# Kernel tuning notes

Measured on AMD Instinct MI355X. Metric: run time of the kernel, lower is better.

Reference implementation:

```python
import jax, jax.numpy as jnp
import numpy as np

DIM = 768
NUM_HEADS = 12
HEAD_DIM = DIM // NUM_HEADS
SCALE = HEAD_DIM ** -0.5


def setup_inputs() -> dict:
    key = jax.random.key(0)
    k1, k2, k3, k4 = jax.random.split(key, 4)
    B, N = 4, 2048
    x = jax.random.normal(k1, (B, N, DIM), dtype=jnp.float32)
    # torch nn.Linear weights: [out_features, in_features]
    w_qkv = jax.random.normal(k2, (3 * DIM, DIM), dtype=jnp.float32) * (DIM ** -0.5)
    w_proj = jax.random.normal(k3, (DIM, DIM), dtype=jnp.float32) * (DIM ** -0.5)
    b_proj = jax.random.normal(k4, (DIM,), dtype=jnp.float32) * 0.01
    return {"x": x, "w_qkv": w_qkv, "w_proj": w_proj, "b_proj": b_proj}


def reference(x, w_qkv, w_proj, b_proj):
    B, N, C = x.shape
    H, D = NUM_HEADS, HEAD_DIM
    qkv = jnp.einsum('bnc,oc->bno', x, w_qkv)              # [B,N,3C]
    qkv = qkv.reshape(B, N, 3, H, D)
    q = qkv[:, :, 0].transpose(0, 2, 1, 3)                 # [B,H,N,D]
    k = qkv[:, :, 1].transpose(0, 2, 1, 3)
    v = qkv[:, :, 2].transpose(0, 2, 1, 3)
    attn = jnp.einsum('bhnd,bhmd->bhnm', q, k) * SCALE     # [B,H,N,N]
    attn = jax.nn.softmax(attn, axis=-1)
    out = jnp.einsum('bhnm,bhmd->bhnd', attn, v)           # [B,H,N,D]
    out = out.transpose(0, 2, 1, 3).reshape(B, N, C)
    return jnp.einsum('bnc,oc->bno', out, w_proj) + b_proj
```

## Files before the change

kernel.cpp:

```cpp
#include <hip/hip_runtime.h>
#include <hip/hip_bf16.h>
#include <cstdint>

typedef _Float16 f16;
typedef __attribute__((ext_vector_type(8))) _Float16 f16x8;
typedef __attribute__((ext_vector_type(4))) _Float16 f16x4;
typedef __attribute__((ext_vector_type(2))) _Float16 f16x2;
typedef __attribute__((ext_vector_type(4))) float f32x4;

#define MFMA(a, b, c) __builtin_amdgcn_mfma_f32_16x16x32_f16((a), (b), (c), 0, 0, 0)
#define MFMA16(a, b, c) __builtin_amdgcn_mfma_f32_16x16x16f16((a), (b), (c), 0, 0, 0)

__device__ static inline void gl_lds16(const void* g, void* l) {
  __builtin_amdgcn_global_load_lds(
      (__attribute__((address_space(1))) const void*)g,
      (__attribute__((address_space(3))) void*)l, 16, 0, 0);
}

__global__ __launch_bounds__(256) void cvt_all(const float* __restrict__ x,
                                               const float* __restrict__ wq,
                                               const float* __restrict__ wp,
                                               f16* __restrict__ xo,
                                               f16* __restrict__ wqo,
                                               f16* __restrict__ wpo) {
  int i = blockIdx.x * 256 + threadIdx.x;
  const float* src;
  f16* dst;
  if (i < 1572864) {
    src = x; dst = xo;
  } else if (i < 1572864 + 442368) {
    i -= 1572864; src = wq; dst = wqo;
  } else {
    i -= 1572864 + 442368;
    if (i >= 147456) return;
    src = wp; dst = wpo;
  }
  const float4 v = reinterpret_cast<const float4*>(src)[i];
  f16x4 o;
  o.x = (f16)v.x; o.y = (f16)v.y; o.z = (f16)v.z; o.w = (f16)v.w;
  reinterpret_cast<f16x4*>(dst)[i] = o;
}

__global__ __launch_bounds__(256) void gemm_qkv(const f16* __restrict__ X,
                                                const f16* __restrict__ W,
                                                f16* __restrict__ Q,
                                                f16* __restrict__ Ko,
                                                f16* __restrict__ Vt) {
  __shared__ f16 As[128 * 64];
  __shared__ f16 Bs[128 * 64];
  const int tid = threadIdx.x;
  const int lane = tid & 63;
  const int w = tid >> 6;
  const int m0 = blockIdx.x * 128;
  const int n0 = blockIdx.y * 128;
  const int wr = (w >> 1) * 64;
  const int wc = (w & 1) * 64;
  const int srow = lane >> 3;
  const int scol = (lane & 7) * 8;
  f32x4 acc[4][4] = {};

  for (int k0 = 0; k0 < 768; k0 += 64) {
#pragma unroll
    for (int i = 0; i < 4; ++i) {
      const int c = w * 4 + i;
      const int row = c * 8 + srow;
      gl_lds16(X + (size_t)(m0 + row) * 768 + k0 + scol, &As[c * 512]);
      gl_lds16(W + (size_t)(n0 + row) * 768 + k0 + scol, &Bs[c * 512]);
    }
    __syncthreads();
#pragma unroll
    for (int kk = 0; kk < 2; ++kk) {
      const int ko = kk * 32 + (lane >> 4) * 8;
      f16x8 af[4], bf[4];
#pragma unroll
      for (int i = 0; i < 4; ++i)
        af[i] = *reinterpret_cast<const f16x8*>(&As[(wr + i * 16 + (lane & 15)) * 64 + ko]);
#pragma unroll
      for (int j = 0; j < 4; ++j)
        bf[j] = *reinterpret_cast<const f16x8*>(&Bs[(wc + j * 16 + (lane & 15)) * 64 + ko]);
#pragma unroll
      for (int i = 0; i < 4; ++i)
#pragma unroll
        for (int j = 0; j < 4; ++j)
          acc[i][j] = MFMA(af[i], bf[j], acc[i][j]);
    }
    __syncthreads();
  }

  const int b = m0 >> 11;
  const int nbase = (m0 & 2047) + wr;
  const int which = n0 / 768;
  const int h = ((n0 % 768) >> 6) + (wc >> 6);
  const float QSCL = 0.125f * 1.44269504088896340736f;
#pragma unroll
  for (int i = 0; i < 4; ++i) {
#pragma unroll
    for (int j = 0; j < 4; ++j) {
      const int d = j * 16 + (lane & 15);
      if (which == 2) {
        f16x4 vv;
#pragma unroll
        for (int r = 0; r < 4; ++r) vv[r] = (f16)acc[i][j][r];
        *reinterpret_cast<f16x4*>(
            &Vt[(((size_t)(b * 12 + h)) * 64 + d) * 2048 + nbase + i * 16 +
                (lane >> 4) * 4]) = vv;
      } else if (which == 0) {
#pragma unroll
        for (int r = 0; r < 4; ++r) {
          const int n = nbase + i * 16 + (lane >> 4) * 4 + r;
          Q[(((size_t)(b * 12 + h)) * 2048 + n) * 64 + d] = (f16)(acc[i][j][r] * QSCL);
        }
      } else {
#pragma unroll
        for (int r = 0; r < 4; ++r) {
          const int n = nbase + i * 16 + (lane >> 4) * 4 + r;
          Ko[(((size_t)(b * 12 + h)) * 2048 + n) * 64 + d] = (f16)acc[i][j][r];
        }
      }
    }
  }
}

__global__ __launch_bounds__(256, 2) void attn_fwd(const f16* __restrict__ Q,
                                                   const f16* __restrict__ K,
                                                   const f16* __restrict__ Vt,
                                                   f16* __restrict__ Ao) {
  __shared__ char smem[49152];
  const int tid = threadIdx.x, lane = tid & 63, w = tid >> 6;
  const int l15 = lane & 15, hi = lane >> 4;
  const int half = tid >> 7;
  const int ptd = tid & 127;

  const int id = blockIdx.x;
  const int sw = (id & 7) * 96 + (id >> 3);
  const int bh = sw >> 4;
  const int qt = sw & 15;
  const int b = bh / 12, h = bh % 12;
  const int q0 = qt * 128 + (w & 1) * 64;
  const f16* Qp = Q + (size_t)bh * 2048 * 64;
  const f16* Kp = K + (size_t)bh * 2048 * 64;
  const f16* Vp = Vt + (size_t)bh * 64 * 2048;

  char* hb = smem + half * 24576;
  const int kvb = half * 1024;

  const int tr = ptd >> 3;
  const int ss = ptd & 7;
  const int ssw = ss ^ (tr & 7);
  const f16* ksrc0 = Kp + (size_t)(kvb + tr) * 64 + ssw * 8;
  const f16* vsrc0 = Vp + (size_t)tr * 2048 + kvb + ssw * 8;
  char* kdst = hb + tr * 128 + ss * 16;
  char* vdst = hb + 16384 + tr * 128 + ss * 16;

  auto stageK = [&](int tt, int bufo) {
#pragma unroll
    for (int i = 0; i < 4; ++i)
      gl_lds16(ksrc0 + (size_t)(tt * 64 + i * 16) * 64, kdst + bufo + i * 2048);
  };
  auto stageV = [&](int tt) {
#pragma unroll
    for (int i = 0; i < 4; ++i)
      gl_lds16(vsrc0 + (size_t)i * 32768 + tt * 64, vdst + i * 2048);
  };

  stageV(0);
  stageK(0, 0);
  stageK(1, 8192);

  f16x8 qf[4][2];
#pragma unroll
  for (int mi = 0; mi < 4; ++mi)
#pragma unroll
    for (int kk = 0; kk < 2; ++kk)
      qf[mi][kk] = *reinterpret_cast<const f16x8*>(
          &Qp[(size_t)(q0 + mi * 16 + l15) * 64 + kk * 32 + hi * 8]);

  const char* kb[2];
#pragma unroll
  for (int kk = 0; kk < 2; ++kk)
    kb[kk] = hb + l15 * 128 + (((kk * 4 + hi) ^ (l15 & 7)) << 4);
  const char* vb[4];
#pragma unroll
  for (int nj = 0; nj < 4; ++nj)
    vb[nj] = hb + 16384 + l15 * 128 +
             ((((nj * 2 + (hi >> 1)) ^ (l15 & 7)) << 4) + (hi & 1) * 8);

  f32x4 o[4][4] = {};
  f32x4 lsv[4] = {};
  const f32x4 Z4 = {0.f, 0.f, 0.f, 0.f};

#pragma unroll 1
  for (int t = 0; t < 16; ++t) {
    if (t < 15) asm volatile("s_waitcnt vmcnt(4)" ::: "memory");
    else        asm volatile("s_waitcnt vmcnt(0)" ::: "memory");
    __builtin_amdgcn_s_barrier();
    const int cbo = (t & 1) * 8192;
    f16x8 kf[4][2];
#pragma unroll
    for (int nj = 0; nj < 4; ++nj)
#pragma unroll
      for (int kk = 0; kk < 2; ++kk)
        kf[nj][kk] = *reinterpret_cast<const f16x8*>(kb[kk] + cbo + nj * 2048);
    f16x4 vf[4][4];
#pragma unroll
    for (int nj = 0; nj < 4; ++nj)
#pragma unroll
      for (int j = 0; j < 4; ++j)
        vf[nj][j] = *reinterpret_cast<const f16x4*>(vb[nj] + j * 2048);
    asm volatile("s_waitcnt lgkmcnt(0)" ::: "memory");
    __builtin_amdgcn_s_barrier();
    if (t < 15) stageV(t + 1);
    if (t < 14) stageK(t + 2, cbo);
    f32x4 s[4][4];
    __builtin_amdgcn_s_setprio(1);
#pragma unroll
    for (int nj = 0; nj < 4; ++nj)
#pragma unroll
      for (int mi = 0; mi < 4; ++mi) {
        s[nj][mi] = MFMA(kf[nj][0], qf[mi][0], Z4);
        s[nj][mi] = MFMA(kf[nj][1], qf[mi][1], s[nj][mi]);
      }
    __builtin_amdgcn_s_setprio(0);
    f16x4 pk[4][4];
#pragma unroll
    for (int nj = 0; nj < 4; ++nj)
#pragma unroll
      for (int mi = 0; mi < 4; ++mi) {
        f32x4 pv;
#pragma unroll
        for (int r = 0; r < 4; ++r) pv[r] = __builtin_amdgcn_exp2f(s[nj][mi][r]);
        lsv[mi] += pv;
        const f16x2 plo = __builtin_bit_cast(f16x2, __builtin_amdgcn_cvt_pkrtz(pv[0], pv[1]));
        const f16x2 phi = __builtin_bit_cast(f16x2, __builtin_amdgcn_cvt_pkrtz(pv[2], pv[3]));
        pk[nj][mi] = __builtin_shufflevector(plo, phi, 0, 1, 2, 3);
      }
    __builtin_amdgcn_s_setprio(1);
#pragma unroll
    for (int nj = 0; nj < 4; ++nj)
#pragma unroll
      for (int j = 0; j < 4; ++j)
#pragma unroll
        for (int mi = 0; mi < 4; ++mi)
          o[j][mi] = MFMA16(vf[nj][j], pk[nj][mi], o[j][mi]);
    __builtin_amdgcn_s_setprio(0);
  }

  __syncthreads();
  if (w >= 2) {
    char* ob = smem + (w - 2) * 16384;
    char* lb = smem + 32768 + (w - 2) * 4096;
#pragma unroll
    for (int j = 0; j < 4; ++j)
#pragma unroll
      for (int mi = 0; mi < 4; ++mi)
        *reinterpret_cast<f32x4*>(ob + (j * 4 + mi) * 1024 + lane * 16) = o[j][mi];
#pragma unroll
    for (int mi = 0; mi < 4; ++mi)
      *reinterpret_cast<f32x4*>(lb + mi * 1024 + lane * 16) = lsv[mi];
  }
  __syncthreads();
  if (w < 2) {
    const char* ob = smem + w * 16384;
    const char* lb = smem + 32768 + w * 4096;
#pragma unroll
    for (int j = 0; j < 4; ++j)
#pragma unroll
      for (int mi = 0; mi < 4; ++mi)
        o[j][mi] += *reinterpret_cast<const f32x4*>(ob + (j * 4 + mi) * 1024 + lane * 16);
#pragma unroll
    for (int mi = 0; mi < 4; ++mi)
      lsv[mi] += *reinterpret_cast<const f32x4*>(lb + mi * 1024 + lane * 16);

    float lt[4];
#pragma unroll
    for (int mi = 0; mi < 4; ++mi) {
      float t = lsv[mi][0] + lsv[mi][1] + lsv[mi][2] + lsv[mi][3];
      t += __shfl_xor(t, 16);
      t += __shfl_xor(t, 32);
      lt[mi] = 1.0f / t;
    }
    asm volatile("s_waitcnt lgkmcnt(0)" ::: "memory");
    __builtin_amdgcn_sched_barrier(0);

    f16* Pw = reinterpret_cast<f16*>(smem + w * 16384);
#pragma unroll
    for (int mi = 0; mi < 4; ++mi)
#pragma unroll
      for (int j = 0; j < 4; ++j) {
        f16x4 ok;
#pragma unroll
        for (int r = 0; r < 4; ++r) ok[r] = (f16)(o[j][mi][r] * lt[mi]);
        *reinterpret_cast<f16x4*>(&Pw[(mi * 16 + l15) * 72 + j * 16 + hi * 4]) = ok;
      }
#pragma unroll
    for (int t = 0; t < 8; ++t) {
      const f16x8 v = *reinterpret_cast<const f16x8*>(&Pw[lane * 72 + t * 8]);
      *reinterpret_cast<f16x8*>(
          &Ao[((size_t)(b * 2048 + q0 + lane)) * 768 + h * 64 + t * 8]) = v;
    }
  }
}

__global__ __launch_bounds__(256) void gemm_proj(const f16* __restrict__ A,
                                                 const f16* __restrict__ W,
                                                 const float* __restrict__ bias,
                                                 float* __restrict__ out) {
  __shared__ f16 As[64 * 64];
  __shared__ f16 Bs[128 * 64];
  const int tid = threadIdx.x;
  const int lane = tid & 63;
  const int w = tid >> 6;
  const int m0 = blockIdx.x * 64;
  const int n0 = blockIdx.y * 128;
  const int wr = (w >> 1) * 32;
  const int wc = (w & 1) * 64;
  const int srow = tid >> 3;
  const int scol = (tid & 7) * 8;
  f32x4 acc[2][4] = {};

  for (int k0 = 0; k0 < 768; k0 += 64) {
#pragma unroll
    for (int i = 0; i < 2; ++i)
      gl_lds16(A + (size_t)(m0 + i * 32 + srow) * 768 + k0 + scol,
               &As[(i * 32 + srow) * 64 + scol]);
#pragma unroll
    for (int i = 0; i < 4; ++i)
      gl_lds16(W + (size_t)(n0 + i * 32 + srow) * 768 + k0 + scol,
               &Bs[(i * 32 + srow) * 64 + scol]);
    __syncthreads();
#pragma unroll
    for (int kk = 0; kk < 2; ++kk) {
      const int ko = kk * 32 + (lane >> 4) * 8;
      f16x8 af[2], bf[4];
#pragma unroll
      for (int i = 0; i < 2; ++i)
        af[i] = *reinterpret_cast<const f16x8*>(&As[(wr + i * 16 + (lane & 15)) * 64 + ko]);
#pragma unroll
      for (int j = 0; j < 4; ++j)
        bf[j] = *reinterpret_cast<const f16x8*>(&Bs[(wc + j * 16 + (lane & 15)) * 64 + ko]);
#pragma unroll
      for (int i = 0; i < 2; ++i)
#pragma unroll
        for (int j = 0; j < 4; ++j)
          acc[i][j] = MFMA(af[i], bf[j], acc[i][j]);
    }
    __syncthreads();
  }

#pragma unroll
  for (int j = 0; j < 4; ++j) {
    const int col = n0 + wc + j * 16 + (lane & 15);
    const float bj = bias[col];
#pragma unroll
    for (int i = 0; i < 2; ++i)
#pragma unroll
      for (int r = 0; r < 4; ++r)
        out[(size_t)(m0 + wr + i * 16 + (lane >> 4) * 4 + r) * 768 + col] =
            acc[i][j][r] + bj;
  }
}

extern "C" void kernel_launch(void* const* d_in, const int* in_sizes, int n_in,
                              void* d_out, int out_size, void* d_ws, size_t ws_size,
                              hipStream_t stream) {
  const float* x      = (const float*)d_in[0];
  const float* w_qkv  = (const float*)d_in[1];
  const float* w_proj = (const float*)d_in[2];
  const float* b_proj = (const float*)d_in[3];
  float* out = (float*)d_out;
  char* ws = (char*)d_ws;

  f16* xh  = (f16*)(ws);
  f16* wqh = (f16*)(ws + 12582912);
  f16* wph = (f16*)(ws + 16121856);
  f16* Qb  = (f16*)(ws + 17301504);
  f16* Kb  = (f16*)(ws + 29884416);
  f16* Vtb = (f16*)(ws + 42467328);
  f16* Ah  = (f16*)(ws + 55050240);

  cvt_all<<<8448, 256, 0, stream>>>(x, w_qkv, w_proj, xh, wqh, wph);
  gemm_qkv<<<dim3(64, 18), 256, 0, stream>>>(xh, wqh, Qb, Kb, Vtb);
  attn_fwd<<<768, 256, 0, stream>>>(Qb, Kb, Vtb, Ah);
  gemm_proj<<<dim3(128, 6), 256, 0, stream>>>(Ah, wph, b_proj, out);
}
```

Measured before the change: 162.3 us.

## Double-buffer GEMM tiles and stage QKV epilogue through LDS for coalesced stores

Both GEMM kernels move to a double-buffered LDS pipeline. The next k-tile is issued with async global-to-LDS loads while the current tile is consumed, and a partial vmcnt wait plus raw barriers replace the full syncthreads. The QKV epilogue now transposes accumulators through LDS so Q, K and V are written with 16-byte coalesced stores instead of scalar 2-byte stores. Q is stored transposed, so the attention kernel now gathers its Q fragments with strided scalar loads, which adds some uncoalesced reads at attention start in exchange for cheaper QKV writes.

Result: faster. 148.9 us (-8.3%).

```diff
diff --git a/kernel.cpp b/kernel.cpp
--- a/kernel.cpp
+++ b/kernel.cpp
@@ -43,14 +43,15 @@
 
 __global__ __launch_bounds__(256) void gemm_qkv(const f16* __restrict__ X,
                                                 const f16* __restrict__ W,
-                                                f16* __restrict__ Q,
+                                                f16* __restrict__ Qt,
                                                 f16* __restrict__ Ko,
                                                 f16* __restrict__ Vt) {
-  __shared__ f16 As[128 * 64];
-  __shared__ f16 Bs[128 * 64];
+  __shared__ f16 As[2][8192];
+  __shared__ f16 Bs[2][8192];
   const int tid = threadIdx.x;
   const int lane = tid & 63;
   const int w = tid >> 6;
+  const int l15 = lane & 15, hi = lane >> 4;
   const int m0 = blockIdx.x * 128;
   const int n0 = blockIdx.y * 128;
   const int wr = (w >> 1) * 64;
@@ -59,69 +60,97 @@
   const int scol = (lane & 7) * 8;
   f32x4 acc[4][4] = {};
 
-  for (int k0 = 0; k0 < 768; k0 += 64) {
+  auto stage = [&](int buf, int k0) {
 #pragma unroll
     for (int i = 0; i < 4; ++i) {
-      const int c = w * 4 + i;
-      const int row = c * 8 + srow;
-      gl_lds16(X + (size_t)(m0 + row) * 768 + k0 + scol, &As[c * 512]);
-      gl_lds16(W + (size_t)(n0 + row) * 768 + k0 + scol, &Bs[c * 512]);
-    }
-    __syncthreads();
+      const int row = (w * 4 + i) * 8 + srow;
+      gl_lds16(X + (size_t)(m0 + row) * 768 + k0 + scol, &As[buf][row * 64 + scol]);
+      gl_lds16(W + (size_t)(n0 + row) * 768 + k0 + scol, &Bs[buf][row * 64 + scol]);
+    }
+  };
+  stage(0, 0);
+  stage(1, 64);
+
+#pragma unroll 1
+  for (int t = 0; t < 12; ++t) {
+    if (t < 11) asm volatile("s_waitcnt vmcnt(8)" ::: "memory");
+    else        asm volatile("s_waitcnt vmcnt(0)" ::: "memory");
+    __builtin_amdgcn_s_barrier();
+    const int cb = t & 1;
 #pragma unroll
     for (int kk = 0; kk < 2; ++kk) {
-      const int ko = kk * 32 + (lane >> 4) * 8;
+      const int ko = kk * 32 + hi * 8;
       f16x8 af[4], bf[4];
 #pragma unroll
       for (int i = 0; i < 4; ++i)
-        af[i] = *reinterpret_cast<const f16x8*>(&As[(wr + i * 16 + (lane & 15)) * 64 + ko]);
+        af[i] = *reinterpret_cast<const f16x8*>(&As[cb][(wr + i * 16 + l15) * 64 + ko]);
 #pragma unroll
       for (int j = 0; j < 4; ++j)
-        bf[j] = *reinterpret_cast<const f16x8*>(&Bs[(wc + j * 16 + (lane & 15)) * 64 + ko]);
+        bf[j] = *reinterpret_cast<const f16x8*>(&Bs[cb][(wc + j * 16 + l15) * 64 + ko]);
 #pragma unroll
       for (int i = 0; i < 4; ++i)
 #pragma unroll
         for (int j = 0; j < 4; ++j)
           acc[i][j] = MFMA(af[i], bf[j], acc[i][j]);
     }
-    __syncthreads();
+    __builtin_amdgcn_s_barrier();
+    if (t < 10) stage(cb, (t + 2) * 64);
   }
 
   const int b = m0 >> 11;
   const int nbase = (m0 & 2047) + wr;
   const int which = n0 / 768;
   const int h = ((n0 % 768) >> 6) + (wc >> 6);
+  const size_t hb = (size_t)(b * 12 + h);
   const float QSCL = 0.125f * 1.44269504088896340736f;
-#pragma unroll
-  for (int i = 0; i < 4; ++i) {
+  f16* T = &As[0][0] + w * 1280;
+
+  if (which != 1) {
+    f16* dst = (which == 2) ? Vt : Qt;
+    const float scl = (which == 0) ? QSCL : 1.0f;
 #pragma unroll
     for (int j = 0; j < 4; ++j) {
-      const int d = j * 16 + (lane & 15);
-      if (which == 2) {
+#pragma unroll
+      for (int i = 0; i < 4; ++i) {
         f16x4 vv;
 #pragma unroll
-        for (int r = 0; r < 4; ++r) vv[r] = (f16)acc[i][j][r];
-        *reinterpret_cast<f16x4*>(
-            &Vt[(((size_t)(b * 12 + h)) * 64 + d) * 2048 + nbase + i * 16 +
-                (lane >> 4) * 4]) = vv;
-      } else if (which == 0) {
-#pragma unroll
-        for (int r = 0; r < 4; ++r) {
-          const int n = nbase + i * 16 + (lane >> 4) * 4 + r;
-          Q[(((size_t)(b * 12 + h)) * 2048 + n) * 64 + d] = (f16)(acc[i][j][r] * QSCL);
-        }
-      } else {
-#pragma unroll
-        for (int r = 0; r < 4; ++r) {
-          const int n = nbase + i * 16 + (lane >> 4) * 4 + r;
-          Ko[(((size_t)(b * 12 + h)) * 2048 + n) * 64 + d] = (f16)acc[i][j][r];
-        }
-      }
-    }
-  }
-}
-
-__global__ __launch_bounds__(256, 2) void attn_fwd(const f16* __restrict__ Q,
+        for (int r = 0; r < 4; ++r) vv[r] = (f16)(acc[i][j][r] * scl);
+        *reinterpret_cast<f16x4*>(&T[l15 * 72 + i * 16 + hi * 4]) = vv;
+      }
+      asm volatile("s_waitcnt lgkmcnt(0)" ::: "memory");
+#pragma unroll
+      for (int t = 0; t < 2; ++t) {
+        const f16x8 v = *reinterpret_cast<const f16x8*>(
+            &T[(t * 8 + (lane >> 3)) * 72 + (lane & 7) * 8]);
+        const int d = j * 16 + t * 8 + (lane >> 3);
+        *reinterpret_cast<f16x8*>(
+            &dst[(hb * 64 + d) * 2048 + nbase + (lane & 7) * 8]) = v;
+      }
+      asm volatile("s_waitcnt lgkmcnt(0)" ::: "memory");
+    }
+  } else {
+#pragma unroll
+    for (int i = 0; i < 4; ++i) {
+#pragma unroll
+      for (int j = 0; j < 4; ++j)
+#pragma unroll
+        for (int r = 0; r < 4; ++r)
+          T[(hi * 4 + r) * 72 + j * 16 + l15] = (f16)acc[i][j][r];
+      asm volatile("s_waitcnt lgkmcnt(0)" ::: "memory");
+#pragma unroll
+      for (int t = 0; t < 2; ++t) {
+        const f16x8 v = *reinterpret_cast<const f16x8*>(
+            &T[(t * 8 + (lane >> 3)) * 72 + (lane & 7) * 8]);
+        const int n = nbase + i * 16 + t * 8 + (lane >> 3);
+        *reinterpret_cast<f16x8*>(
+            &Ko[(hb * 2048 + n) * 64 + (lane & 7) * 8]) = v;
+      }
+      asm volatile("s_waitcnt lgkmcnt(0)" ::: "memory");
+    }
+  }
+}
+
+__global__ __launch_bounds__(256, 2) void attn_fwd(const f16* __restrict__ Qt,
                                                    const f16* __restrict__ K,
                                                    const f16* __restrict__ Vt,
                                                    f16* __restrict__ Ao) {
@@ -137,11 +166,11 @@
   const int qt = sw & 15;
   const int b = bh / 12, h = bh % 12;
   const int q0 = qt * 128 + (w & 1) * 64;
-  const f16* Qp = Q + (size_t)bh * 2048 * 64;
+  const f16* Qp = Qt + (size_t)bh * 64 * 2048;
   const f16* Kp = K + (size_t)bh * 2048 * 64;
   const f16* Vp = Vt + (size_t)bh * 64 * 2048;
 
-  char* hb = smem + half * 24576;
+  char* hbm = smem + half * 24576;
   const int kvb = half * 1024;
 
   const int tr = ptd >> 3;
@@ -149,8 +178,8 @@
   const int ssw = ss ^ (tr & 7);
   const f16* ksrc0 = Kp + (size_t)(kvb + tr) * 64 + ssw * 8;
   const f16* vsrc0 = Vp + (size_t)tr * 2048 + kvb + ssw * 8;
-  char* kdst = hb + tr * 128 + ss * 16;
-  char* vdst = hb + 16384 + tr * 128 + ss * 16;
+  char* kdst = hbm + tr * 128 + ss * 16;
+  char* vdst = hbm + 16384 + tr * 128 + ss * 16;
 
   auto stageK = [&](int tt, int bufo) {
 #pragma unroll
@@ -171,18 +200,22 @@
 #pragma unroll
   for (int mi = 0; mi < 4; ++mi)
 #pragma unroll
-    for (int kk = 0; kk < 2; ++kk)
-      qf[mi][kk] = *reinterpret_cast<const f16x8*>(
-          &Qp[(size_t)(q0 + mi * 16 + l15) * 64 + kk * 32 + hi * 8]);
+    for (int kk = 0; kk < 2; ++kk) {
+      f16x8 v;
+#pragma unroll
+      for (int e = 0; e < 8; ++e)
+        v[e] = Qp[(size_t)(kk * 32 + hi * 8 + e) * 2048 + q0 + mi * 16 + l15];
+      qf[mi][kk] = v;
+    }
 
   const char* kb[2];
 #pragma unroll
   for (int kk = 0; kk < 2; ++kk)
-    kb[kk] = hb + l15 * 128 + (((kk * 4 + hi) ^ (l15 & 7)) << 4);
+    kb[kk] = hbm + l15 * 128 + (((kk * 4 + hi) ^ (l15 & 7)) << 4);
   const char* vb[4];
 #pragma unroll
   for (int nj = 0; nj < 4; ++nj)
-    vb[nj] = hb + 16384 + l15 * 128 +
+    vb[nj] = hbm + 16384 + l15 * 128 +
              ((((nj * 2 + (hi >> 1)) ^ (l15 & 7)) << 4) + (hi & 1) * 8);
 
   f32x4 o[4][4] = {};
@@ -305,8 +338,8 @@
                                                  const f16* __restrict__ W,
                                                  const float* __restrict__ bias,
                                                  float* __restrict__ out) {
-  __shared__ f16 As[64 * 64];
-  __shared__ f16 Bs[128 * 64];
+  __shared__ f16 As[2][4096];
+  __shared__ f16 Bs[2][8192];
   const int tid = threadIdx.x;
   const int lane = tid & 63;
   const int w = tid >> 6;
@@ -318,33 +351,43 @@
   const int scol = (tid & 7) * 8;
   f32x4 acc[2][4] = {};
 
-  for (int k0 = 0; k0 < 768; k0 += 64) {
+  auto stage = [&](int buf, int k0) {
 #pragma unroll
     for (int i = 0; i < 2; ++i)
       gl_lds16(A + (size_t)(m0 + i * 32 + srow) * 768 + k0 + scol,
-               &As[(i * 32 + srow) * 64 + scol]);
+               &As[buf][(i * 32 + srow) * 64 + scol]);
 #pragma unroll
     for (int i = 0; i < 4; ++i)
       gl_lds16(W + (size_t)(n0 + i * 32 + srow) * 768 + k0 + scol,
-               &Bs[(i * 32 + srow) * 64 + scol]);
-    __syncthreads();
+               &Bs[buf][(i * 32 + srow) * 64 + scol]);
+  };
+  stage(0, 0);
+  stage(1, 64);
+
+#pragma unroll 1
+  for (int t = 0; t < 12; ++t) {
+    if (t < 11) asm volatile("s_waitcnt vmcnt(6)" ::: "memory");
+    else        asm volatile("s_waitcnt vmcnt(0)" ::: "memory");
+    __builtin_amdgcn_s_barrier();
+    const int cb = t & 1;
 #pragma unroll
     for (int kk = 0; kk < 2; ++kk) {
       const int ko = kk * 32 + (lane >> 4) * 8;
       f16x8 af[2], bf[4];
 #pragma unroll
       for (int i = 0; i < 2; ++i)
-        af[i] = *reinterpret_cast<const f16x8*>(&As[(wr + i * 16 + (lane & 15)) * 64 + ko]);
+        af[i] = *reinterpret_cast<const f16x8*>(&As[cb][(wr + i * 16 + (lane & 15)) * 64 + ko]);
 #pragma unroll
       for (int j = 0; j < 4; ++j)
-        bf[j] = *reinterpret_cast<const f16x8*>(&Bs[(wc + j * 16 + (lane & 15)) * 64 + ko]);
+        bf[j] = *reinterpret_cast<const f16x8*>(&Bs[cb][(wc + j * 16 + (lane & 15)) * 64 + ko]);
 #pragma unroll
       for (int i = 0; i < 2; ++i)
 #pragma unroll
         for (int j = 0; j < 4; ++j)
           acc[i][j] = MFMA(af[i], bf[j], acc[i][j]);
     }
-    __syncthreads();
+    __builtin_amdgcn_s_barrier();
+    if (t < 10) stage(cb, (t + 2) * 64);
   }
 
 #pragma unroll
@@ -373,13 +416,13 @@
   f16* xh  = (f16*)(ws);
   f16* wqh = (f16*)(ws + 12582912);
   f16* wph = (f16*)(ws + 16121856);
-  f16* Qb  = (f16*)(ws + 17301504);
+  f16* Qtb = (f16*)(ws + 17301504);
   f16* Kb  = (f16*)(ws + 29884416);
   f16* Vtb = (f16*)(ws + 42467328);
   f16* Ah  = (f16*)(ws + 55050240);
 
   cvt_all<<<8448, 256, 0, stream>>>(x, w_qkv, w_proj, xh, wqh, wph);
-  gemm_qkv<<<dim3(64, 18), 256, 0, stream>>>(xh, wqh, Qb, Kb, Vtb);
-  attn_fwd<<<768, 256, 0, stream>>>(Qb, Kb, Vtb, Ah);
+  gemm_qkv<<<dim3(64, 18), 256, 0, stream>>>(xh, wqh, Qtb, Kb, Vtb);
+  attn_fwd<<<768, 256, 0, stream>>>(Qtb, Kb, Vtb, Ah);
   gemm_proj<<<dim3(128, 6), 256, 0, stream>>>(Ah, wph, b_proj, out);
 }
```
